# Kernel tuning notes

Measured on AMD Instinct MI355X. Metric: run time of the kernel, lower is better.

## Reference

```python
import jax, jax.numpy as jnp
import numpy as np

B, S, D = 2, 2048, 1024
H, HD = 16, 64  # num_attention_heads, attention_head_size


def setup_inputs() -> dict:
    key = jax.random.key(0)
    ks = jax.random.split(key, 8)
    std = 0.02
    return {
        "hidden_states": jax.random.normal(ks[0], (B, S, D), dtype=jnp.float32),
        "attention_mask": jnp.zeros((B, 1, 1, S), dtype=jnp.float32),
        "Wq": jax.random.normal(ks[1], (D, D), dtype=jnp.float32) * std,
        "bq": jnp.zeros((D,), dtype=jnp.float32),
        "Wk": jax.random.normal(ks[2], (D, D), dtype=jnp.float32) * std,
        "bk": jnp.zeros((D,), dtype=jnp.float32),
        "Wv": jax.random.normal(ks[3], (D, D), dtype=jnp.float32) * std,
        "bv": jnp.zeros((D,), dtype=jnp.float32),
    }


def reference(hidden_states, attention_mask, Wq, bq, Wk, bk, Wv, bv):
    b, s, d = hidden_states.shape

    def split_heads(x):  # [b,s,D] -> [b,H,s,HD]
        return x.reshape(b, s, H, HD).transpose(0, 2, 1, 3)

    q = split_heads(hidden_states @ Wq + bq)
    k = split_heads(hidden_states @ Wk + bk)
    v = split_heads(hidden_states @ Wv + bv)

    scores = jnp.einsum("bhqd,bhkd->bhqk", q, k) / jnp.sqrt(jnp.float32(HD))
    scores = scores + attention_mask  # additive mask, broadcast [b,1,1,s]
    probs = jax.nn.softmax(scores, axis=-1)  # dropout is identity at inference
    ctx = jnp.einsum("bhqk,bhkd->bhqd", probs, v)
    out = ctx.transpose(0, 2, 1, 3).reshape(b, s, d)
    return out
```

## Files before the change

### kernel.cpp

```cpp
#include <hip/hip_runtime.h>
#include <math.h>

#define CB 2
#define CS 2048
#define CD 1024
#define CH 16
#define CHD 64
#define CM (CB*CS)

#define QSCALE 0.18033688f
#define LOG2E  1.44269504f
#define BLOG   40.0f

typedef unsigned short u16;
using bf16x8 = __attribute__((ext_vector_type(8))) short;
using u16x8  = __attribute__((ext_vector_type(8))) unsigned short;
using f32x4  = __attribute__((ext_vector_type(4))) float;

__device__ __forceinline__ u16 f2bf(float f) {
    unsigned int u = __float_as_uint(f);
    u = (u + 0x7FFFu + ((u >> 16) & 1u)) >> 16;
    return (u16)u;
}

__device__ __forceinline__ unsigned cvt_pk_bf16(float lo, float hi) {
    unsigned r;
    asm("v_cvt_pk_bf16_f32 %0, %1, %2" : "=v"(r) : "v"(lo), "v"(hi));
    return r;
}

__device__ __forceinline__ void load_lds16(const u16* g, u16* l) {
    __builtin_amdgcn_global_load_lds(
        (const __attribute__((address_space(1))) unsigned int*)g,
        (__attribute__((address_space(3))) unsigned int*)l, 16, 0, 0);
}

__global__ __launch_bounds__(256)
void convert_x(const float* __restrict__ X, u16* __restrict__ Xb)
{
    size_t i = ((size_t)blockIdx.x * 256 + threadIdx.x) * 8;
    float4 v0 = *(const float4*)(X + i);
    float4 v1 = *(const float4*)(X + i + 4);
    u16x8 o;
    o[0] = f2bf(v0.x); o[1] = f2bf(v0.y); o[2] = f2bf(v0.z); o[3] = f2bf(v0.w);
    o[4] = f2bf(v1.x); o[5] = f2bf(v1.y); o[6] = f2bf(v1.z); o[7] = f2bf(v1.w);
    *(u16x8*)(Xb + i) = o;
}

__global__ __launch_bounds__(256)
void convert_wt(const float* __restrict__ Wq, const float* __restrict__ Wk,
                const float* __restrict__ Wv, u16* __restrict__ Wt)
{
    const int z = blockIdx.z;
    const float* W = (z == 0) ? Wq : (z == 1) ? Wk : Wv;
    const float sc = (z == 0) ? QSCALE : 1.0f;
    u16* Wo = Wt + (size_t)z * CD * CD;

    __shared__ u16 T[64][72];
    const int k0 = blockIdx.x << 6;
    const int n0 = blockIdx.y << 6;
    const int tid = threadIdx.x;

    #pragma unroll
    for (int it = 0; it < 4; ++it) {
        int r = (tid >> 4) + (it << 4);
        int c = (tid & 15) << 2;
        float4 v = *(const float4*)(W + (size_t)(k0 + r) * CD + n0 + c);
        T[c + 0][r] = f2bf(v.x * sc);
        T[c + 1][r] = f2bf(v.y * sc);
        T[c + 2][r] = f2bf(v.z * sc);
        T[c + 3][r] = f2bf(v.w * sc);
    }
    __syncthreads();
    #pragma unroll
    for (int it = 0; it < 2; ++it) {
        int cc = tid + (it << 8);
        int n  = cc >> 3;
        int ch = (cc & 7) << 3;
        *(uint4*)(Wo + (size_t)(n0 + n) * CD + k0 + ch) = *(const uint4*)&T[n][ch];
    }
}

__global__ __launch_bounds__(256, 3)
void qkv_gemm_mfma(const u16* __restrict__ Xb, const u16* __restrict__ Wt,
                   const float* __restrict__ bq, const float* __restrict__ bk,
                   const float* __restrict__ bv,
                   u16* __restrict__ Qb, u16* __restrict__ Kb,
                   u16* __restrict__ Vt)
{
    const int z = blockIdx.z;
    const u16* W = Wt + (size_t)z * CD * CD;
    const float* bias = (z == 0) ? bq : (z == 1) ? bk : bv;
    const float bscale = (z == 0) ? QSCALE : 1.0f;

    __shared__ u16 smem[16384];
    u16* As = smem;
    u16* Bs = smem + 8192;

    const int tid  = threadIdx.x;
    const int w    = tid >> 6;
    const int l    = tid & 63;
    const int l15  = l & 15;
    const int quad = l >> 4;
    const int wm   = w >> 1;
    const int wn   = w & 1;

    const int row0 = blockIdx.x << 7;
    const int n0   = blockIdx.y << 7;

    f32x4 acc[4][4];
    #pragma unroll
    for (int mi = 0; mi < 4; ++mi)
        #pragma unroll
        for (int nt = 0; nt < 4; ++nt)
            acc[mi][nt] = (f32x4){0.f, 0.f, 0.f, 0.f};

    const u16* Ag = Xb + (size_t)row0 * CD;
    const u16* Bg = W  + (size_t)n0   * CD;
    const int lr8 = l >> 3;
    const int ls  = l & 7;
    const int lg  = (ls ^ lr8) << 3;
    const int q7  = l15 & 7;

    for (int k0 = 0; k0 < CD; k0 += 64) {
        __syncthreads();
        #pragma unroll
        for (int i = 0; i < 4; ++i) {
            int r = w * 32 + 8 * i + lr8;
            load_lds16(Ag + (size_t)r * CD + k0 + lg, As + (size_t)(w * 32 + 8 * i) * 64);
            load_lds16(Bg + (size_t)r * CD + k0 + lg, Bs + (size_t)(w * 32 + 8 * i) * 64);
        }
        __syncthreads();

        #pragma unroll
        for (int kk = 0; kk < 2; ++kk) {
            bf16x8 af[4], bfr[4];
            #pragma unroll
            for (int mi = 0; mi < 4; ++mi)
                af[mi] = *(const bf16x8*)
                    &As[(wm * 64 + mi * 16 + l15) * 64 + (((kk * 4 + quad) ^ q7) << 3)];
            #pragma unroll
            for (int nt = 0; nt < 4; ++nt)
                bfr[nt] = *(const bf16x8*)
                    &Bs[(wn * 64 + nt * 16 + l15) * 64 + (((kk * 4 + quad) ^ q7) << 3)];
            #pragma unroll
            for (int mi = 0; mi < 4; ++mi)
                #pragma unroll
                for (int nt = 0; nt < 4; ++nt)
                    acc[mi][nt] = __builtin_amdgcn_mfma_f32_16x16x32_bf16(
                        af[mi], bfr[nt], acc[mi][nt], 0, 0, 0);
        }
    }

    __syncthreads();

    if (z < 2) {
        u16* Og = (z == 0) ? Qb : Kb;
        float bb[4];
        #pragma unroll
        for (int nt = 0; nt < 4; ++nt)
            bb[nt] = bias[n0 + wn * 64 + nt * 16 + l15] * bscale;

        u16 (*Ct)[136] = (u16(*)[136])smem;
        #pragma unroll
        for (int mh = 0; mh < 2; ++mh) {
            if (wm == mh) {
                #pragma unroll
                for (int nt = 0; nt < 4; ++nt)
                    #pragma unroll
                    for (int mi = 0; mi < 4; ++mi)
                        #pragma unroll
                        for (int r = 0; r < 4; ++r)
                            Ct[mi * 16 + quad * 4 + r][wn * 64 + nt * 16 + l15] =
                                f2bf(acc[mi][nt][r] + bb[nt]);
            }
            __syncthreads();
            #pragma unroll
            for (int it = 0; it < 4; ++it) {
                int c  = tid + (it << 8);
                int rl = c >> 4;
                int ck = c & 15;
                uint4 d = *(const uint4*)&Ct[rl][ck * 8];
                int gcol = n0 + ck * 8;
                int h = gcol >> 6, hd = gcol & 63;
                int m = row0 + mh * 64 + rl;
                int b = m >> 11, s = m & (CS - 1);
                *(uint4*)(Og + ((size_t)(b * CH + h) * CS + s) * CHD + hd) = d;
            }
            __syncthreads();
        }
    } else {
        u16 (*Ct)[136] = (u16(*)[136])smem;
        #pragma unroll
        for (int nh = 0; nh < 2; ++nh) {
            if (wn == nh) {
                #pragma unroll
                for (int nt = 0; nt < 4; ++nt) {
                    int col = n0 + nh * 64 + nt * 16 + l15;
                    float bb = bias[col];
                    #pragma unroll
                    for (int mi = 0; mi < 4; ++mi)
                        #pragma unroll
                        for (int r = 0; r < 4; ++r) {
                            int ml = wm * 64 + mi * 16 + quad * 4 + r;
                            Ct[nt * 16 + l15][ml] = f2bf(acc[mi][nt][r] + bb);
                        }
                }
            }
            __syncthreads();
            #pragma unroll
            for (int it = 0; it < 4; ++it) {
                int c   = tid + (it << 8);
                int dvl = c >> 4;
                int ch  = c & 15;
                uint4 vdat = *(const uint4*)&Ct[dvl][ch * 8];
                int col = n0 + nh * 64 + dvl;
                int h   = col >> 6;
                int dv  = col & 63;
                int m0  = row0 + ch * 8;
                int b   = m0 >> 11;
                int s0  = m0 & (CS - 1);
                *(uint4*)(Vt + (((size_t)(b * CH + h)) * CHD + dv) * CS + s0) = vdat;
            }
            __syncthreads();
        }
    }
}


#define AT_TILE(KT, MVC, MVN)                                                 \
    {                                                                         \
        const int k0 = (KT) << 6;                                             \
        __syncthreads();                                                      \
        _Pragma("unroll")                                                     \
        for (int i = 0; i < 2; ++i) {                                         \
            int rl = qh * 16 + 8 * i;                                         \
            load_lds16(Kph + (size_t)(k0 + rl + lr8) * CHD + lg, &Kst[rl * 64]); \
            load_lds16(Vph + (size_t)(rl + lr8) * CS + k0 + lg,  &Vst[rl * 64]); \
        }                                                                     \
        __syncthreads();                                                      \
        bf16x8 kf[4][2];                                                      \
        _Pragma("unroll")                                                     \
        for (int mt = 0; mt < 4; ++mt)                                        \
            _Pragma("unroll")                                                 \
            for (int hh = 0; hh < 2; ++hh)                                    \
                kf[mt][hh] = *(const bf16x8*)                                 \
                    &Kst[(mt * 16 + l15) * 64 + (((hh * 4 + quad) ^ q7) << 3)]; \
        const int kn = ((KT) + 1) & 15;                                       \
        _Pragma("unroll")                                                     \
        for (int mt = 0; mt < 4; ++mt)                                        \
            MVN[mt] = *(const f32x4*)(mrh + (kn << 6) + mt * 16 + quad * 4);  \
        f32x4 mc[4];                                                          \
        _Pragma("unroll")                                                     \
        for (int mt = 0; mt < 4; ++mt)                                        \
            _Pragma("unroll")                                                 \
            for (int r = 0; r < 4; ++r)                                       \
                mc[mt][r] = fmaf(MVC[mt][r], LOG2E, -BLOG);                   \
        _Pragma("unroll")                                                     \
        for (int nq = 0; nq < 2; ++nq) {                                      \
            f32x4 st[4];                                                      \
            _Pragma("unroll")                                                 \
            for (int mt = 0; mt < 4; ++mt) {                                  \
                f32x4 c0 = mc[mt];                                            \
                c0 = __builtin_amdgcn_mfma_f32_16x16x32_bf16(kf[mt][0], qf[nq][0], c0, 0, 0, 0); \
                st[mt] = __builtin_amdgcn_mfma_f32_16x16x32_bf16(kf[mt][1], qf[nq][1], c0, 0, 0, 0); \
            }                                                                 \
            _Pragma("unroll")                                                 \
            for (int mt = 0; mt < 4; ++mt) {                                  \
                _Pragma("unroll")                                             \
                for (int r = 0; r < 4; ++r) st[mt][r] = exp2f(st[mt][r]);     \
                int g = 2 * mt + (quad >> 1);                                 \
                int addr = (nq * 16 + l15) * 64 + ((g ^ q7) << 3) + ((quad & 1) << 2); \
                uint2 d;                                                      \
                d.x = cvt_pk_bf16(st[mt][0], st[mt][1]);                      \
                d.y = cvt_pk_bf16(st[mt][2], st[mt][3]);                      \
                *(uint2*)&Pw[addr] = d;                                       \
            }                                                                 \
        }                                                                     \
        bf16x8 pf[2][2];                                                      \
        _Pragma("unroll")                                                     \
        for (int nq = 0; nq < 2; ++nq)                                        \
            _Pragma("unroll")                                                 \
            for (int hh = 0; hh < 2; ++hh)                                    \
                pf[nq][hh] = *(const bf16x8*)                                 \
                    &Pw[(nq * 16 + l15) * 64 + (((hh * 4 + quad) ^ q7) << 3)]; \
        bf16x8 vf[4][2];                                                      \
        _Pragma("unroll")                                                     \
        for (int dt = 0; dt < 4; ++dt)                                        \
            _Pragma("unroll")                                                 \
            for (int hh = 0; hh < 2; ++hh)                                    \
                vf[dt][hh] = *(const bf16x8*)                                 \
                    &Vst[(dt * 16 + l15) * 64 + (((hh * 4 + quad) ^ q7) << 3)]; \
        _Pragma("unroll")                                                     \
        for (int nq = 0; nq < 2; ++nq) {                                      \
            Lq[nq] = __builtin_amdgcn_mfma_f32_16x16x32_bf16(pf[nq][0], ones, Lq[nq], 0, 0, 0); \
            Lq[nq] = __builtin_amdgcn_mfma_f32_16x16x32_bf16(pf[nq][1], ones, Lq[nq], 0, 0, 0); \
            _Pragma("unroll")                                                 \
            for (int dt = 0; dt < 4; ++dt) {                                  \
                O[nq][dt] = __builtin_amdgcn_mfma_f32_16x16x32_bf16(          \
                    pf[nq][0], vf[dt][0], O[nq][dt], 0, 0, 0);                \
                O[nq][dt] = __builtin_amdgcn_mfma_f32_16x16x32_bf16(          \
                    pf[nq][1], vf[dt][1], O[nq][dt], 0, 0, 0);                \
            }                                                                 \
        }                                                                     \
    }

__global__ __launch_bounds__(512, 4)
void attn_mfma(const u16* __restrict__ Qg, const u16* __restrict__ Kg,
               const u16* __restrict__ Vtg, const float* __restrict__ mask,
               float* __restrict__ out)
{
    __shared__ u16 smem[32768];
    u16* KstB = smem;
    u16* VstB = smem + 8192;
    u16* PlB  = smem + 16384;

    const int flat = blockIdx.y * 16 + blockIdx.x;
    const int nf   = ((flat & 7) << 6) + (flat >> 3);
    const int q0   = (nf & 15) << 7;
    const int bh   = nf >> 4;
    const int b    = bh >> 4;
    const int h    = bh & 15;

    const int tid = threadIdx.x;
    const int w    = tid >> 6;
    const int qh   = w & 3;
    const int kh   = w >> 2;
    const int l    = tid & 63;
    const int l15  = l & 15;
    const int quad = l >> 4;
    const int q7   = l15 & 7;
    const int lr8  = l >> 3;
    const int lg   = ((l & 7) ^ lr8) << 3;

    const u16* Qp     = Qg  + (size_t)bh * CS * CHD;
    const u16* Kph    = Kg  + (size_t)bh * CS * CHD + ((size_t)(kh << 10)) * CHD;
    const u16* Vph    = Vtg + (size_t)bh * CHD * CS + (kh << 10);
    const float* mrh  = mask + (size_t)b * CS + (kh << 10);

    u16* Kst = KstB + kh * 4096;
    u16* Vst = VstB + kh * 4096;
    u16* Pw  = PlB  + w * 2048;

    bf16x8 qf[2][2];
    #pragma unroll
    for (int nq = 0; nq < 2; ++nq)
        #pragma unroll
        for (int hh = 0; hh < 2; ++hh)
            qf[nq][hh] = *(const bf16x8*)(
                Qp + (size_t)(q0 + qh * 32 + nq * 16 + l15) * CHD + hh * 32 + quad * 8);

    const short ob16 = (short)0x3F80;
    const bf16x8 ones = {ob16, ob16, ob16, ob16, ob16, ob16, ob16, ob16};

    f32x4 Lq[2];
    Lq[0] = (f32x4){0.f, 0.f, 0.f, 0.f};
    Lq[1] = (f32x4){0.f, 0.f, 0.f, 0.f};
    f32x4 O[2][4];
    #pragma unroll
    for (int nq = 0; nq < 2; ++nq)
        #pragma unroll
        for (int dt = 0; dt < 4; ++dt)
            O[nq][dt] = (f32x4){0.f, 0.f, 0.f, 0.f};

    f32x4 mvA[4], mvB[4];
    #pragma unroll
    for (int mt = 0; mt < 4; ++mt)
        mvA[mt] = *(const f32x4*)(mrh + mt * 16 + quad * 4);

    #pragma unroll 1
    for (int kt = 0; kt < 16; kt += 2) {
        AT_TILE(kt,     mvA, mvB)
        AT_TILE(kt + 1, mvB, mvA)
    }

    float lsum[2];
    #pragma unroll
    for (int nq = 0; nq < 2; ++nq) {
        const int src = (l15 >> 2) << 4;
        float s0 = __shfl(Lq[nq][0], src);
        float s1 = __shfl(Lq[nq][1], src);
        float s2 = __shfl(Lq[nq][2], src);
        float s3 = __shfl(Lq[nq][3], src);
        float lo = (l15 & 1) ? s1 : s0;
        float hi2 = (l15 & 1) ? s3 : s2;
        lsum[nq] = (l15 & 2) ? hi2 : lo;
    }

    __syncthreads();
    float* ob   = (float*)smem;
    float* lbuf = (float*)PlB;

    if (kh == 1) {
        float* obw = ob + qh * 2048;
        #pragma unroll
        for (int nq = 0; nq < 2; ++nq)
            #pragma unroll
            for (int dt = 0; dt < 4; ++dt)
                #pragma unroll
                for (int r = 0; r < 4; ++r)
                    obw[(nq * 16 + quad * 4 + r) * 64 + dt * 16 + l15] = O[nq][dt][r];
        if (quad == 0) {
            lbuf[qh * 32 + l15]      = lsum[0];
            lbuf[qh * 32 + 16 + l15] = lsum[1];
        }
    }
    __syncthreads();

    if (kh == 0) {
        const float* obw = ob + qh * 2048;
        #pragma unroll
        for (int nq = 0; nq < 2; ++nq) {
            float inv = 1.0f / (lsum[nq] + lbuf[qh * 32 + nq * 16 + l15]);
            #pragma unroll
            for (int r = 0; r < 4; ++r) {
                float invr = __shfl(inv, quad * 4 + r);
                int q = q0 + qh * 32 + nq * 16 + quad * 4 + r;
                float* orow = out + ((size_t)b * CS + q) * CD + h * CHD;
                #pragma unroll
                for (int dt = 0; dt < 4; ++dt)
                    orow[dt * 16 + l15] =
                        (O[nq][dt][r] + obw[(nq * 16 + quad * 4 + r) * 64 + dt * 16 + l15]) * invr;
            }
        }
    }
}

extern "C" void kernel_launch(void* const* d_in, const int* in_sizes, int n_in,
                              void* d_out, int out_size, void* d_ws, size_t ws_size,
                              hipStream_t stream)
{
    const float* X    = (const float*)d_in[0];
    const float* mask = (const float*)d_in[1];
    const float* Wq   = (const float*)d_in[2];
    const float* bq   = (const float*)d_in[3];
    const float* Wk   = (const float*)d_in[4];
    const float* bk   = (const float*)d_in[5];
    const float* Wv   = (const float*)d_in[6];
    const float* bv   = (const float*)d_in[7];
    float* out = (float*)d_out;

    char* ws = (char*)d_ws;
    u16* Xb = (u16*)(ws);
    u16* Wt = (u16*)(ws + ((size_t)8  << 20));
    u16* Qb = (u16*)(ws + ((size_t)14 << 20));
    u16* Kb = (u16*)(ws + ((size_t)22 << 20));
    u16* Vt = (u16*)(ws + ((size_t)30 << 20));

    convert_x<<<CM * CD / (256 * 8), 256, 0, stream>>>(X, Xb);
    convert_wt<<<dim3(16, 16, 3), 256, 0, stream>>>(Wq, Wk, Wv, Wt);
    qkv_gemm_mfma<<<dim3(CM / 128, CD / 128, 3), 256, 0, stream>>>(
        Xb, Wt, bq, bk, bv, Qb, Kb, Vt);
    attn_mfma<<<dim3(CS / 128, CB * CH), 512, 0, stream>>>(Qb, Kb, Vt, mask, out);
}
```

Measured before the change: 185.1 us.

## Double-buffer K tiles in LDS and compute row sums with VALU adds

K tiles are double-buffered in LDS: the next K tile is prefetched while the current one is used, and one of the two barriers per tile is moved to just before the V fragment reads. Row sums of P are now accumulated with scalar adds plus a cross-quad xor shuffle, replacing the extra MFMAs against a ones vector. The mask is added inside the exp2 argument instead of being preloaded into the MFMA accumulator, and the per-wave P scratch is halved by reusing one 16-row slot. This adds VALU work and a different barrier placement, and it risks LDS hazards if the prefetch into the alternate buffer overlaps with readers.

After: 280.1 us. +51.3%, slower.

```diff
diff --git a/kernel.cpp b/kernel.cpp
--- a/kernel.cpp
+++ b/kernel.cpp
@@ -228,62 +228,61 @@
 }
 
 
-#define AT_TILE(KT, MVC, MVN)                                                 \
+#define AT_TILE(KT, KC, KN)                                                   \
     {                                                                         \
         const int k0 = (KT) << 6;                                             \
-        __syncthreads();                                                      \
+        __syncthreads();        \
         _Pragma("unroll")                                                     \
         for (int i = 0; i < 2; ++i) {                                         \
             int rl = qh * 16 + 8 * i;                                         \
-            load_lds16(Kph + (size_t)(k0 + rl + lr8) * CHD + lg, &Kst[rl * 64]); \
-            load_lds16(Vph + (size_t)(rl + lr8) * CS + k0 + lg,  &Vst[rl * 64]); \
+            load_lds16(Vph + (size_t)(rl + lr8) * CS + k0 + lg, &Vst[rl * 64]); \
+            if ((KT) < 15)                                                    \
+                load_lds16(Kph + (size_t)(k0 + 64 + rl + lr8) * CHD + lg,     \
+                           &(KN)[rl * 64]);                                   \
         }                                                                     \
-        __syncthreads();                                                      \
+        f32x4 mv[4];                                                          \
+        _Pragma("unroll")                                                     \
+        for (int mt = 0; mt < 4; ++mt)                                        \
+            mv[mt] = *(const f32x4*)(mrh + k0 + mt * 16 + quad * 4);          \
         bf16x8 kf[4][2];                                                      \
         _Pragma("unroll")                                                     \
         for (int mt = 0; mt < 4; ++mt)                                        \
             _Pragma("unroll")                                                 \
             for (int hh = 0; hh < 2; ++hh)                                    \
                 kf[mt][hh] = *(const bf16x8*)                                 \
-                    &Kst[(mt * 16 + l15) * 64 + (((hh * 4 + quad) ^ q7) << 3)]; \
-        const int kn = ((KT) + 1) & 15;                                       \
-        _Pragma("unroll")                                                     \
-        for (int mt = 0; mt < 4; ++mt)                                        \
-            MVN[mt] = *(const f32x4*)(mrh + (kn << 6) + mt * 16 + quad * 4);  \
-        f32x4 mc[4];                                                          \
-        _Pragma("unroll")                                                     \
-        for (int mt = 0; mt < 4; ++mt)                                        \
-            _Pragma("unroll")                                                 \
-            for (int r = 0; r < 4; ++r)                                       \
-                mc[mt][r] = fmaf(MVC[mt][r], LOG2E, -BLOG);                   \
+                    &(KC)[(mt * 16 + l15) * 64 + (((hh * 4 + quad) ^ q7) << 3)]; \
+        bf16x8 pf[2][2];                                                      \
         _Pragma("unroll")                                                     \
         for (int nq = 0; nq < 2; ++nq) {                                      \
             f32x4 st[4];                                                      \
             _Pragma("unroll")                                                 \
             for (int mt = 0; mt < 4; ++mt) {                                  \
-                f32x4 c0 = mc[mt];                                            \
+                f32x4 c0 = (f32x4){-BLOG, -BLOG, -BLOG, -BLOG};               \
                 c0 = __builtin_amdgcn_mfma_f32_16x16x32_bf16(kf[mt][0], qf[nq][0], c0, 0, 0, 0); \
                 st[mt] = __builtin_amdgcn_mfma_f32_16x16x32_bf16(kf[mt][1], qf[nq][1], c0, 0, 0, 0); \
             }                                                                 \
+            float rs = lsum[nq];                                              \
             _Pragma("unroll")                                                 \
             for (int mt = 0; mt < 4; ++mt) {                                  \
                 _Pragma("unroll")                                             \
-                for (int r = 0; r < 4; ++r) st[mt][r] = exp2f(st[mt][r]);     \
+                for (int r = 0; r < 4; ++r) {                                 \
+                    st[mt][r] = exp2f(fmaf(mv[mt][r], LOG2E, st[mt][r]));     \
+                    rs += st[mt][r];                                          \
+                }                                                             \
                 int g = 2 * mt + (quad >> 1);                                 \
-                int addr = (nq * 16 + l15) * 64 + ((g ^ q7) << 3) + ((quad & 1) << 2); \
+                int addr = l15 * 64 + ((g ^ q7) << 3) + ((quad & 1) << 2);    \
                 uint2 d;                                                      \
                 d.x = cvt_pk_bf16(st[mt][0], st[mt][1]);                      \
                 d.y = cvt_pk_bf16(st[mt][2], st[mt][3]);                      \
                 *(uint2*)&Pw[addr] = d;                                       \
             }                                                                 \
-        }                                                                     \
-        bf16x8 pf[2][2];                                                      \
-        _Pragma("unroll")                                                     \
-        for (int nq = 0; nq < 2; ++nq)                                        \
+            lsum[nq] = rs;                                                    \
             _Pragma("unroll")                                                 \
             for (int hh = 0; hh < 2; ++hh)                                    \
                 pf[nq][hh] = *(const bf16x8*)                                 \
-                    &Pw[(nq * 16 + l15) * 64 + (((hh * 4 + quad) ^ q7) << 3)]; \
+                    &Pw[l15 * 64 + (((hh * 4 + quad) ^ q7) << 3)];            \
+        }                                                                     \
+        __syncthreads();          \
         bf16x8 vf[4][2];                                                      \
         _Pragma("unroll")                                                     \
         for (int dt = 0; dt < 4; ++dt)                                        \
@@ -292,9 +291,7 @@
                 vf[dt][hh] = *(const bf16x8*)                                 \
                     &Vst[(dt * 16 + l15) * 64 + (((hh * 4 + quad) ^ q7) << 3)]; \
         _Pragma("unroll")                                                     \
-        for (int nq = 0; nq < 2; ++nq) {                                      \
-            Lq[nq] = __builtin_amdgcn_mfma_f32_16x16x32_bf16(pf[nq][0], ones, Lq[nq], 0, 0, 0); \
-            Lq[nq] = __builtin_amdgcn_mfma_f32_16x16x32_bf16(pf[nq][1], ones, Lq[nq], 0, 0, 0); \
+        for (int nq = 0; nq < 2; ++nq)                                        \
             _Pragma("unroll")                                                 \
             for (int dt = 0; dt < 4; ++dt) {                                  \
                 O[nq][dt] = __builtin_amdgcn_mfma_f32_16x16x32_bf16(          \
@@ -302,7 +299,6 @@
                 O[nq][dt] = __builtin_amdgcn_mfma_f32_16x16x32_bf16(          \
                     pf[nq][1], vf[dt][1], O[nq][dt], 0, 0, 0);                \
             }                                                                 \
-        }                                                                     \
     }
 
 __global__ __launch_bounds__(512, 4)
@@ -311,9 +307,6 @@
                float* __restrict__ out)
 {
     __shared__ u16 smem[32768];
-    u16* KstB = smem;
-    u16* VstB = smem + 8192;
-    u16* PlB  = smem + 16384;
 
     const int flat = blockIdx.y * 16 + blockIdx.x;
     const int nf   = ((flat & 7) << 6) + (flat >> 3);
@@ -338,9 +331,10 @@
     const u16* Vph    = Vtg + (size_t)bh * CHD * CS + (kh << 10);
     const float* mrh  = mask + (size_t)b * CS + (kh << 10);
 
-    u16* Kst = KstB + kh * 4096;
-    u16* Vst = VstB + kh * 4096;
-    u16* Pw  = PlB  + w * 2048;
+    u16* KstA = smem + kh * 8192;
+    u16* KstB = KstA + 4096;
+    u16* Vst  = smem + 16384 + kh * 4096;
+    u16* Pw   = smem + 24576 + w * 1024;
 
     bf16x8 qf[2][2];
     #pragma unroll
@@ -350,12 +344,7 @@
             qf[nq][hh] = *(const bf16x8*)(
                 Qp + (size_t)(q0 + qh * 32 + nq * 16 + l15) * CHD + hh * 32 + quad * 8);
 
-    const short ob16 = (short)0x3F80;
-    const bf16x8 ones = {ob16, ob16, ob16, ob16, ob16, ob16, ob16, ob16};
-
-    f32x4 Lq[2];
-    Lq[0] = (f32x4){0.f, 0.f, 0.f, 0.f};
-    Lq[1] = (f32x4){0.f, 0.f, 0.f, 0.f};
+    float lsum[2] = {0.f, 0.f};
     f32x4 O[2][4];
     #pragma unroll
     for (int nq = 0; nq < 2; ++nq)
@@ -363,33 +352,27 @@
         for (int dt = 0; dt < 4; ++dt)
             O[nq][dt] = (f32x4){0.f, 0.f, 0.f, 0.f};
 
-    f32x4 mvA[4], mvB[4];
-    #pragma unroll
-    for (int mt = 0; mt < 4; ++mt)
-        mvA[mt] = *(const f32x4*)(mrh + mt * 16 + quad * 4);
+    #pragma unroll
+    for (int i = 0; i < 2; ++i) {
+        int rl = qh * 16 + 8 * i;
+        load_lds16(Kph + (size_t)(rl + lr8) * CHD + lg, &KstA[rl * 64]);
+    }
 
     #pragma unroll 1
     for (int kt = 0; kt < 16; kt += 2) {
-        AT_TILE(kt,     mvA, mvB)
-        AT_TILE(kt + 1, mvB, mvA)
-    }
-
-    float lsum[2];
+        AT_TILE(kt,     KstA, KstB)
+        AT_TILE(kt + 1, KstB, KstA)
+    }
+
     #pragma unroll
     for (int nq = 0; nq < 2; ++nq) {
-        const int src = (l15 >> 2) << 4;
-        float s0 = __shfl(Lq[nq][0], src);
-        float s1 = __shfl(Lq[nq][1], src);
-        float s2 = __shfl(Lq[nq][2], src);
-        float s3 = __shfl(Lq[nq][3], src);
-        float lo = (l15 & 1) ? s1 : s0;
-        float hi2 = (l15 & 1) ? s3 : s2;
-        lsum[nq] = (l15 & 2) ? hi2 : lo;
+        lsum[nq] += __shfl_xor(lsum[nq], 16);
+        lsum[nq] += __shfl_xor(lsum[nq], 32);
     }
 
     __syncthreads();
     float* ob   = (float*)smem;
-    float* lbuf = (float*)PlB;
+    float* lbuf = (float*)(smem + 16384);
 
     if (kh == 1) {
         float* obw = ob + qh * 2048;
```
